# Kernel tuning notes

Measured on AMD Instinct MI355X. Metric: run time of the kernel, lower is better.

## Reference

```python
import jax, jax.numpy as jnp
import numpy as np

B, S, H = 8, 1024, 1024
NH, DH = 16, 64
F_DIM, E, TOPK = 4096, 8, 2
EPS = 1e-5


def setup_inputs() -> dict:
    key = jax.random.key(0)
    ks = jax.random.split(key, 12)
    s = 0.02
    return {
        "x": jax.random.normal(ks[0], (B, S, H), jnp.float32),
        "ln1_w": jnp.ones((H,), jnp.float32),
        "ln1_b": jnp.zeros((H,), jnp.float32),
        "ln2_w": jnp.ones((H,), jnp.float32),
        "ln2_b": jnp.zeros((H,), jnp.float32),
        "in_proj_w": jax.random.normal(ks[1], (3 * H, H), jnp.float32) * s,
        "in_proj_b": jnp.zeros((3 * H,), jnp.float32),
        "out_proj_w": jax.random.normal(ks[2], (H, H), jnp.float32) * s,
        "out_proj_b": jnp.zeros((H,), jnp.float32),
        "gate_w": jax.random.normal(ks[3], (E, H), jnp.float32) * s,
        "gate_b": jnp.zeros((E,), jnp.float32),
        "w1": jax.random.normal(ks[4], (E, H, F_DIM), jnp.float32) * s,
        "b1": jnp.zeros((E, F_DIM), jnp.float32),
        "w2": jax.random.normal(ks[5], (E, F_DIM, H), jnp.float32) * s,
        "b2": jnp.zeros((E, H), jnp.float32),
    }


def _layernorm(x, w, b):
    mu = jnp.mean(x, axis=-1, keepdims=True)
    var = jnp.var(x, axis=-1, keepdims=True)
    return (x - mu) * jax.lax.rsqrt(var + EPS) * w + b


def reference(x, ln1_w, ln1_b, ln2_w, ln2_b, in_proj_w, in_proj_b,
              out_proj_w, out_proj_b, gate_w, gate_b, w1, b1, w2, b2):
    # --- attention sub-block ---
    xn = _layernorm(x, ln1_w, ln1_b)
    qkv = xn @ in_proj_w.T + in_proj_b                     # [B,S,3H]
    q, k, v = jnp.split(qkv, 3, axis=-1)
    q = q.reshape(B, S, NH, DH).transpose(0, 2, 1, 3)      # [B,NH,S,DH]
    k = k.reshape(B, S, NH, DH).transpose(0, 2, 1, 3)
    v = v.reshape(B, S, NH, DH).transpose(0, 2, 1, 3)
    scores = jnp.einsum("bhqd,bhkd->bhqk", q, k) / jnp.sqrt(jnp.float32(DH))
    attn = jax.nn.softmax(scores, axis=-1)
    ctx = jnp.einsum("bhqk,bhkd->bhqd", attn, v)
    ctx = ctx.transpose(0, 2, 1, 3).reshape(B, S, H)
    x = x + ctx @ out_proj_w.T + out_proj_b

    # --- MoE sub-block (dense compute-all-experts, top-k combine) ---
    xn2 = _layernorm(x, ln2_w, ln2_b)
    logits = xn2 @ gate_w.T + gate_b                       # [B,S,E]
    topk_vals, topk_idx = jax.lax.top_k(logits, TOPK)      # [B,S,K]
    probs = jax.nn.softmax(topk_vals, axis=-1)
    hid = jax.nn.gelu(jnp.einsum("bsh,ehf->bsef", xn2, w1) + b1, approximate=False)
    expert_out = jnp.einsum("bsef,efh->bseh", hid, w2) + b2  # [B,S,E,H]
    selected = jnp.take_along_axis(expert_out, topk_idx[..., None], axis=2)  # [B,S,K,H]
    moe_out = jnp.sum(probs[..., None] * selected, axis=2)
    return x + moe_out
```

## Files before the change

kernel.cpp:

```cpp
#include <hip/hip_runtime.h>
#include <math.h>

typedef unsigned short u16;
typedef short short8 __attribute__((ext_vector_type(8)));
typedef float f32x4 __attribute__((ext_vector_type(4)));
typedef unsigned short us4 __attribute__((ext_vector_type(4)));

#define NTOK 8192
#define NEXP 8

__device__ __forceinline__ u16 f2bf(float f) {
  union { float f; unsigned u; } v; v.f = f;
  unsigned r = v.u + 0x7FFFu + ((v.u >> 16) & 1u);
  return (u16)(r >> 16);
}

__global__ void cast_kernel(const float* __restrict__ in, u16* __restrict__ out, int n4) {
  int i = blockIdx.x * blockDim.x + threadIdx.x;
  if (i < n4) {
    float4 v = ((const float4*)in)[i];
    us4 o;
    o[0] = f2bf(v.x); o[1] = f2bf(v.y); o[2] = f2bf(v.z); o[3] = f2bf(v.w);
    ((us4*)out)[i] = o;
  }
}

__global__ void transpose_cast(const float* __restrict__ in, u16* __restrict__ out, int R, int C) {
  __shared__ float tile[32][33];
  const size_t eoff = (size_t)blockIdx.z * (size_t)R * (size_t)C;
  in += eoff; out += eoff;
  int tx = threadIdx.x & 31, ty = threadIdx.x >> 5;
  int rb = blockIdx.y * 32, cb = blockIdx.x * 32;
#pragma unroll
  for (int p = 0; p < 4; ++p)
    tile[ty + p*8][tx] = in[(size_t)(rb + ty + p*8) * C + (cb + tx)];
  __syncthreads();
#pragma unroll
  for (int p = 0; p < 4; ++p)
    out[(size_t)(cb + ty + p*8) * R + (rb + tx)] = f2bf(tile[tx][ty + p*8]);
}

__global__ void ln1_kernel(const float* __restrict__ x, const float* __restrict__ w,
                           const float* __restrict__ b, u16* __restrict__ xn) {
  const int t = blockIdx.x, tid = threadIdx.x;
  __shared__ float red[8];
  float4 v = ((const float4*)(x + (size_t)t * 1024))[tid];
  float s  = v.x + v.y + v.z + v.w;
  float sq = v.x*v.x + v.y*v.y + v.z*v.z + v.w*v.w;
#pragma unroll
  for (int m = 1; m < 64; m <<= 1) { s += __shfl_xor(s, m, 64); sq += __shfl_xor(sq, m, 64); }
  if ((tid & 63) == 0) { red[tid >> 6] = s; red[4 + (tid >> 6)] = sq; }
  __syncthreads();
  float S = red[0] + red[1] + red[2] + red[3];
  float Q = red[4] + red[5] + red[6] + red[7];
  float mu  = S * (1.0f / 1024.0f);
  float var = Q * (1.0f / 1024.0f) - mu * mu;
  float inv = rsqrtf(var + 1e-5f);
  float4 wv = ((const float4*)w)[tid];
  float4 bv = ((const float4*)b)[tid];
  us4 o;
  o[0] = f2bf((v.x - mu) * inv * wv.x + bv.x);
  o[1] = f2bf((v.y - mu) * inv * wv.y + bv.y);
  o[2] = f2bf((v.z - mu) * inv * wv.z + bv.z);
  o[3] = f2bf((v.w - mu) * inv * wv.w + bv.w);
  ((us4*)(xn + (size_t)t * 1024))[tid] = o;
}

__global__ void ln2_gate_kernel(const float* __restrict__ x2, const float* __restrict__ w,
                                const float* __restrict__ b, const float* __restrict__ gw,
                                const float* __restrict__ gb, u16* __restrict__ xn2,
                                int* __restrict__ cnt, int* __restrict__ list_tok,
                                float* __restrict__ list_prob) {
  const int t = blockIdx.x, tid = threadIdx.x;
  __shared__ float red[8];
  __shared__ float logits[NEXP];
  __shared__ float xrow[1024];
  float4 v = ((const float4*)(x2 + (size_t)t * 1024))[tid];
  float s  = v.x + v.y + v.z + v.w;
  float sq = v.x*v.x + v.y*v.y + v.z*v.z + v.w*v.w;
#pragma unroll
  for (int m = 1; m < 64; m <<= 1) { s += __shfl_xor(s, m, 64); sq += __shfl_xor(sq, m, 64); }
  if ((tid & 63) == 0) { red[tid >> 6] = s; red[4 + (tid >> 6)] = sq; }
  __syncthreads();
  float S = red[0] + red[1] + red[2] + red[3];
  float Q = red[4] + red[5] + red[6] + red[7];
  float mu  = S * (1.0f / 1024.0f);
  float var = Q * (1.0f / 1024.0f) - mu * mu;
  float inv = rsqrtf(var + 1e-5f);
  float4 wv = ((const float4*)w)[tid];
  float4 bv = ((const float4*)b)[tid];
  float n0 = (v.x - mu) * inv * wv.x + bv.x;
  float n1 = (v.y - mu) * inv * wv.y + bv.y;
  float n2 = (v.z - mu) * inv * wv.z + bv.z;
  float n3 = (v.w - mu) * inv * wv.w + bv.w;
  xrow[tid*4+0] = n0; xrow[tid*4+1] = n1; xrow[tid*4+2] = n2; xrow[tid*4+3] = n3;
  us4 o; o[0] = f2bf(n0); o[1] = f2bf(n1); o[2] = f2bf(n2); o[3] = f2bf(n3);
  ((us4*)(xn2 + (size_t)t * 1024))[tid] = o;
  __syncthreads();
  int e = tid >> 5, l32 = tid & 31;
  const float* gwe = gw + e * 1024;
  float part = 0.0f;
  for (int i = l32; i < 1024; i += 32) part += xrow[i] * gwe[i];
#pragma unroll
  for (int m = 1; m < 32; m <<= 1) part += __shfl_xor(part, m, 64);
  if (l32 == 0) logits[e] = part + gb[e];
  __syncthreads();
  if (tid == 0) {
    float v0 = -1e30f; int e0 = 0;
#pragma unroll
    for (int i = 0; i < NEXP; ++i) { float L = logits[i]; if (L > v0) { v0 = L; e0 = i; } }
    float v1 = -1e30f; int e1 = 0;
#pragma unroll
    for (int i = 0; i < NEXP; ++i) { if (i == e0) continue; float L = logits[i]; if (L > v1) { v1 = L; e1 = i; } }
    float texp = expf(v1 - v0);
    float p0 = 1.0f / (1.0f + texp);
    float p1 = texp / (1.0f + texp);
    int s0 = atomicAdd(&cnt[e0], 1);
    list_tok[e0 * NTOK + s0] = t; list_prob[e0 * NTOK + s0] = p0;
    int s1 = atomicAdd(&cnt[e1], 1);
    list_tok[e1 * NTOK + s1] = t; list_prob[e1 * NTOK + s1] = p1;
  }
}

__launch_bounds__(256)
__global__ void attn_kernel(const u16* __restrict__ qkv, u16* __restrict__ ctx) {
  const int bh = blockIdx.y;
  const int b = bh >> 4, h = bh & 15;
  const int q0 = blockIdx.x * 64;
  const int tokBase = b * 1024;
  __shared__ __align__(16) u16 Qs[64 * 72];
  __shared__ __align__(16) u16 Ks[64 * 72];
  __shared__ __align__(16) u16 Vts[64 * 72];
  __shared__ __align__(16) u16 Ps[64 * 72];
  const int tid = threadIdx.x;
  const int wave = tid >> 6, lane = tid & 63, g = lane >> 4, lr = lane & 15;

  {
    int r = tid >> 2, d0 = (tid & 3) * 16;
    const u16* src = qkv + (size_t)(tokBase + q0 + r) * 3072 + h * 64 + d0;
    *(short8*)&Qs[r * 72 + d0]     = *(const short8*)src;
    *(short8*)&Qs[r * 72 + d0 + 8] = *(const short8*)(src + 8);
  }
  __syncthreads();
  short8 aq0 = *(const short8*)&Qs[(wave * 16 + lr) * 72 + g * 8];
  short8 aq1 = *(const short8*)&Qs[(wave * 16 + lr) * 72 + 32 + g * 8];

  const f32x4 zf = {0.f, 0.f, 0.f, 0.f};
  f32x4 Ofr[4] = {zf, zf, zf, zf};
  float m_run[4], l_run[4];
#pragma unroll
  for (int r = 0; r < 4; ++r) { m_run[r] = -1e30f; l_run[r] = 0.f; }

  for (int kt = 0; kt < 1024; kt += 64) {
    __syncthreads();
    {
      int r = tid >> 2, d0 = (tid & 3) * 16;
      const u16* ksrc = qkv + (size_t)(tokBase + kt + r) * 3072 + 1024 + h * 64 + d0;
      *(short8*)&Ks[r * 72 + d0]     = *(const short8*)ksrc;
      *(short8*)&Ks[r * 72 + d0 + 8] = *(const short8*)(ksrc + 8);
      const u16* vsrc = qkv + (size_t)(tokBase + kt + r) * 3072 + 2048 + h * 64 + d0;
      short8 v0 = *(const short8*)vsrc, v1 = *(const short8*)(vsrc + 8);
#pragma unroll
      for (int j = 0; j < 8; ++j) Vts[(d0 + j) * 72 + r] = (u16)v0[j];
#pragma unroll
      for (int j = 0; j < 8; ++j) Vts[(d0 + 8 + j) * 72 + r] = (u16)v1[j];
    }
    __syncthreads();
    f32x4 sf[4];
#pragma unroll
    for (int n = 0; n < 4; ++n) sf[n] = zf;
#pragma unroll
    for (int n = 0; n < 4; ++n) {
      short8 bk0 = *(const short8*)&Ks[(n * 16 + lr) * 72 + g * 8];
      short8 bk1 = *(const short8*)&Ks[(n * 16 + lr) * 72 + 32 + g * 8];
      sf[n] = __builtin_amdgcn_mfma_f32_16x16x32_bf16(aq0, bk0, sf[n], 0, 0, 0);
      sf[n] = __builtin_amdgcn_mfma_f32_16x16x32_bf16(aq1, bk1, sf[n], 0, 0, 0);
    }
#pragma unroll
    for (int n = 0; n < 4; ++n)
#pragma unroll
      for (int r = 0; r < 4; ++r) sf[n][r] *= 0.125f;
    float mnew[4], sc[4];
#pragma unroll
    for (int r = 0; r < 4; ++r) {
      float t0 = fmaxf(fmaxf(sf[0][r], sf[1][r]), fmaxf(sf[2][r], sf[3][r]));
#pragma unroll
      for (int msk = 1; msk < 16; msk <<= 1) t0 = fmaxf(t0, __shfl_xor(t0, msk, 64));
      mnew[r] = fmaxf(m_run[r], t0);
      sc[r] = __expf(m_run[r] - mnew[r]);
      m_run[r] = mnew[r];
    }
#pragma unroll
    for (int n = 0; n < 4; ++n)
#pragma unroll
      for (int r = 0; r < 4; ++r) sf[n][r] = __expf(sf[n][r] - mnew[r]);
#pragma unroll
    for (int r = 0; r < 4; ++r) {
      float s0 = sf[0][r] + sf[1][r] + sf[2][r] + sf[3][r];
#pragma unroll
      for (int msk = 1; msk < 16; msk <<= 1) s0 += __shfl_xor(s0, msk, 64);
      l_run[r] = l_run[r] * sc[r] + s0;
    }
#pragma unroll
    for (int nd = 0; nd < 4; ++nd)
#pragma unroll
      for (int r = 0; r < 4; ++r) Ofr[nd][r] *= sc[r];
#pragma unroll
    for (int n = 0; n < 4; ++n)
#pragma unroll
      for (int r = 0; r < 4; ++r)
        Ps[(wave * 16 + g * 4 + r) * 72 + n * 16 + lr] = f2bf(sf[n][r]);
    __syncthreads();
    short8 ap0 = *(const short8*)&Ps[(wave * 16 + lr) * 72 + g * 8];
    short8 ap1 = *(const short8*)&Ps[(wave * 16 + lr) * 72 + 32 + g * 8];
#pragma unroll
    for (int nd = 0; nd < 4; ++nd) {
      short8 bv0 = *(const short8*)&Vts[(nd * 16 + lr) * 72 + g * 8];
      short8 bv1 = *(const short8*)&Vts[(nd * 16 + lr) * 72 + 32 + g * 8];
      Ofr[nd] = __builtin_amdgcn_mfma_f32_16x16x32_bf16(ap0, bv0, Ofr[nd], 0, 0, 0);
      Ofr[nd] = __builtin_amdgcn_mfma_f32_16x16x32_bf16(ap1, bv1, Ofr[nd], 0, 0, 0);
    }
  }
#pragma unroll
  for (int nd = 0; nd < 4; ++nd)
#pragma unroll
    for (int r = 0; r < 4; ++r) {
      int tok = tokBase + q0 + wave * 16 + g * 4 + r;
      int col = h * 64 + nd * 16 + lr;
      ctx[(size_t)tok * 1024 + col] = f2bf(Ofr[nd][r] / l_run[r]);
    }
}

template<int EPI>
__launch_bounds__(256)
__global__ void gemm128(const u16* __restrict__ Abase, const u16* __restrict__ Bbase,
                        int K, int lda, int N, int ldc,
                        const float* __restrict__ bias,
                        const float* __restrict__ resid,
                        float* __restrict__ outF,
                        u16* __restrict__ outB,
                        const int* __restrict__ cnt,
                        const int* __restrict__ list_tok,
                        const float* __restrict__ list_prob) {
  const int tid = threadIdx.x;
  const int wave = tid >> 6, lane = tid & 63, g = lane >> 4, lr = lane & 15;
  const int n0 = blockIdx.x * 128;
  const int m0 = blockIdx.y * 128;
  const int e  = blockIdx.z;

  int M = NTOK;
  int slotBase = 0;
  const u16* Bw = Bbase;
  const float* biasp = bias;
  if constexpr (EPI == 2 || EPI == 3) {
    for (int j = 0; j < e; ++j) slotBase += cnt[j];
    M = cnt[e];
    if (m0 >= M) return;
    Bw += (size_t)e * (size_t)N * (size_t)K;
    biasp = bias + (size_t)e * N;
  }

  __shared__ __align__(16) u16 As[128 * 64];
  __shared__ __align__(16) u16 Bs[128 * 64];
  char* AsB = (char*)As;
  char* BsB = (char*)Bs;

  size_t aOff[4], bOff[4];
#pragma unroll
  for (int i = 0; i < 4; ++i) {
    int grp = i * 256 + tid;
    int r = grp >> 3;
    int ce = (grp & 7) * 8;
    int arow;
    if constexpr (EPI == 2) {
      int ridx = m0 + r; if (ridx > M - 1) ridx = M - 1;
      arow = list_tok[e * NTOK + ridx];
    } else if constexpr (EPI == 3) {
      int ridx = m0 + r; if (ridx > M - 1) ridx = M - 1;
      arow = slotBase + ridx;
    } else {
      arow = m0 + r;
    }
    aOff[i] = (size_t)arow * (size_t)lda + (size_t)ce;
    bOff[i] = (size_t)(n0 + r) * (size_t)K + (size_t)ce;
  }

  const f32x4 zf = {0.f, 0.f, 0.f, 0.f};
  f32x4 acc[4][4];
#pragma unroll
  for (int m = 0; m < 4; ++m)
#pragma unroll
    for (int n = 0; n < 4; ++n) acc[m][n] = zf;

  const int wm = wave >> 1, wn = wave & 1;

  for (int kt = 0; kt < K; kt += 64) {
#pragma unroll
    for (int i = 0; i < 4; ++i)
      __builtin_amdgcn_global_load_lds(
        (const __attribute__((address_space(1))) unsigned int*)(const void*)(Abase + aOff[i] + kt),
        (__attribute__((address_space(3))) unsigned int*)(void*)(AsB + (i * 256 + wave * 64) * 16),
        16, 0, 0);
#pragma unroll
    for (int i = 0; i < 4; ++i)
      __builtin_amdgcn_global_load_lds(
        (const __attribute__((address_space(1))) unsigned int*)(const void*)(Bw + bOff[i] + kt),
        (__attribute__((address_space(3))) unsigned int*)(void*)(BsB + (i * 256 + wave * 64) * 16),
        16, 0, 0);
    __syncthreads();
    short8 af[4][2], bfr[4][2];
#pragma unroll
    for (int m = 0; m < 4; ++m)
#pragma unroll
      for (int kk = 0; kk < 2; ++kk)
        af[m][kk] = *(const short8*)&As[(wm * 64 + m * 16 + lr) * 64 + kk * 32 + g * 8];
#pragma unroll
    for (int n = 0; n < 4; ++n)
#pragma unroll
      for (int kk = 0; kk < 2; ++kk)
        bfr[n][kk] = *(const short8*)&Bs[(wn * 64 + n * 16 + lr) * 64 + kk * 32 + g * 8];
#pragma unroll
    for (int kk = 0; kk < 2; ++kk)
#pragma unroll
      for (int m = 0; m < 4; ++m)
#pragma unroll
        for (int n = 0; n < 4; ++n)
          acc[m][n] = __builtin_amdgcn_mfma_f32_16x16x32_bf16(af[m][kk], bfr[n][kk], acc[m][n], 0, 0, 0);
    __syncthreads();
  }

#pragma unroll
  for (int m = 0; m < 4; ++m) {
    int rloc = wm * 64 + m * 16 + g * 4;
#pragma unroll
    for (int n = 0; n < 4; ++n) {
      int gc = n0 + wn * 64 + n * 16 + lr;
      float bcol = biasp[gc];
#pragma unroll
      for (int r = 0; r < 4; ++r) {
        int ridx = m0 + rloc + r;
        float vv = acc[m][n][r] + bcol;
        if constexpr (EPI == 0) {
          outB[(size_t)ridx * ldc + gc] = f2bf(vv);
        } else if constexpr (EPI == 1) {
          size_t off = (size_t)ridx * ldc + gc;
          outF[off] = vv + resid[off];
        } else if constexpr (EPI == 2) {
          if (ridx < M)
            outB[(size_t)(slotBase + ridx) * ldc + gc] =
              f2bf(0.5f * vv * (1.0f + erff(vv * 0.70710678f)));
        } else {
          if (ridx < M) {
            int tok = list_tok[e * NTOK + ridx];
            float p = list_prob[e * NTOK + ridx];
            atomicAdd(&outF[(size_t)tok * ldc + gc], vv * p);
          }
        }
      }
    }
  }
}

extern "C" void kernel_launch(void* const* d_in, const int* in_sizes, int n_in,
                              void* d_out, int out_size, void* d_ws, size_t ws_size,
                              hipStream_t stream) {
  const float* x    = (const float*)d_in[0];
  const float* ln1w = (const float*)d_in[1];
  const float* ln1b = (const float*)d_in[2];
  const float* ln2w = (const float*)d_in[3];
  const float* ln2b = (const float*)d_in[4];
  const float* inw  = (const float*)d_in[5];
  const float* inb  = (const float*)d_in[6];
  const float* outw = (const float*)d_in[7];
  const float* outb = (const float*)d_in[8];
  const float* gw   = (const float*)d_in[9];
  const float* gb   = (const float*)d_in[10];
  const float* w1   = (const float*)d_in[11];
  const float* b1   = (const float*)d_in[12];
  const float* w2   = (const float*)d_in[13];
  const float* b2   = (const float*)d_in[14];
  float* out = (float*)d_out;
  char* ws = (char*)d_ws;

  u16* xn1 = (u16*)(ws + 0);
  u16* qkv = (u16*)(ws + 16777216);
  u16* ctx = (u16*)(ws + 67108864);
  u16* hid = (u16*)(ws + 0);
  u16* xn2 = (u16*)(ws + 134217728);
  u16* w1t = (u16*)(ws + 150994944);
  u16* winb  = (u16*)(ws + 218103808);
  u16* woutb = (u16*)(ws + 224395264);
  int*   cnt  = (int*)(ws + 226492416);
  int*   ltok = (int*)(ws + 226492672);
  float* lprb = (float*)(ws + 226754816);
  bool lateW2 = ws_size < 294125824ull;
  u16* w2t = lateW2 ? (u16*)(ws + 134217728) : (u16*)(ws + 227016960);

  cast_kernel<<<3072, 256, 0, stream>>>(inw, winb, 786432);
  cast_kernel<<<1024, 256, 0, stream>>>(outw, woutb, 262144);
  transpose_cast<<<dim3(128, 32, 8), 256, 0, stream>>>(w1, w1t, 1024, 4096);
  if (!lateW2) transpose_cast<<<dim3(32, 128, 8), 256, 0, stream>>>(w2, w2t, 4096, 1024);

  ln1_kernel<<<8192, 256, 0, stream>>>(x, ln1w, ln1b, xn1);
  gemm128<0><<<dim3(24, 64, 1), 256, 0, stream>>>(xn1, winb, 1024, 1024, 3072, 3072,
                                                  inb, nullptr, nullptr, qkv, nullptr, nullptr, nullptr);
  attn_kernel<<<dim3(16, 128), 256, 0, stream>>>(qkv, ctx);
  gemm128<1><<<dim3(8, 64, 1), 256, 0, stream>>>(ctx, woutb, 1024, 1024, 1024, 1024,
                                                 outb, x, out, nullptr, nullptr, nullptr, nullptr);

  hipMemsetAsync(cnt, 0, 32, stream);
  ln2_gate_kernel<<<8192, 256, 0, stream>>>(out, ln2w, ln2b, gw, gb, xn2, cnt, ltok, lprb);
  gemm128<2><<<dim3(32, 64, 8), 256, 0, stream>>>(xn2, w1t, 1024, 1024, 4096, 4096,
                                                  b1, nullptr, nullptr, hid, cnt, ltok, lprb);
  if (lateW2) transpose_cast<<<dim3(32, 128, 8), 256, 0, stream>>>(w2, w2t, 4096, 1024);
  gemm128<3><<<dim3(8, 64, 8), 256, 0, stream>>>(hid, w2t, 4096, 4096, 1024, 1024,
                                                 b2, nullptr, out, nullptr, cnt, ltok, lprb);
}
```

Before: 1.317 ms.

## Use 256x256 double-buffered GEMM tiles, XCD remap, and atomic-free MoE combine

The 128x128 single-buffered GEMM becomes a 256x256 tile, 512-thread kernel. It adds double-buffered LDS stages with global_load_lds prefetching, XOR-swizzled LDS layout, s_setprio around MFMA bursts, and a workgroup remap that groups neighbouring tiles onto the same XCD. The weight transpose now uses 64x64 tiles with vectorized reads and writes. When workspace allows, the second expert GEMM writes bf16 partial outputs that a combine kernel reduces per token using a token-to-slot map, replacing float atomics on the output. The larger tiles raise register and LDS pressure, and the combine adds an extra pass and bf16 rounding of expert outputs.

```diff
diff --git a/kernel.cpp b/kernel.cpp
--- a/kernel.cpp
+++ b/kernel.cpp
@@ -13,6 +13,14 @@
   union { float f; unsigned u; } v; v.f = f;
   unsigned r = v.u + 0x7FFFu + ((v.u >> 16) & 1u);
   return (u16)(r >> 16);
+}
+__device__ __forceinline__ float bf2f(u16 u) {
+  union { unsigned u; float f; } v; v.u = ((unsigned)u) << 16; return v.f;
+}
+__device__ __forceinline__ void gload16(const u16* src, u16* ldsDst) {
+  __builtin_amdgcn_global_load_lds(
+    (const __attribute__((address_space(1))) unsigned int*)(const void*)src,
+    (__attribute__((address_space(3))) unsigned int*)(void*)ldsDst, 16, 0, 0);
 }
 
 __global__ void cast_kernel(const float* __restrict__ in, u16* __restrict__ out, int n4) {
@@ -26,18 +34,32 @@
 }
 
 __global__ void transpose_cast(const float* __restrict__ in, u16* __restrict__ out, int R, int C) {
-  __shared__ float tile[32][33];
+  __shared__ float tile[64][65];
   const size_t eoff = (size_t)blockIdx.z * (size_t)R * (size_t)C;
   in += eoff; out += eoff;
-  int tx = threadIdx.x & 31, ty = threadIdx.x >> 5;
-  int rb = blockIdx.y * 32, cb = blockIdx.x * 32;
-#pragma unroll
-  for (int p = 0; p < 4; ++p)
-    tile[ty + p*8][tx] = in[(size_t)(rb + ty + p*8) * C + (cb + tx)];
-  __syncthreads();
-#pragma unroll
-  for (int p = 0; p < 4; ++p)
-    out[(size_t)(cb + ty + p*8) * R + (rb + tx)] = f2bf(tile[tx][ty + p*8]);
+  const int rb = blockIdx.y * 64, cb = blockIdx.x * 64;
+  const int tid = threadIdx.x;
+  const int lr4 = tid >> 4;
+  const int lc4 = (tid & 15) * 4;
+#pragma unroll
+  for (int p = 0; p < 4; ++p) {
+    float4 v = *(const float4*)&in[(size_t)(rb + p * 16 + lr4) * C + cb + lc4];
+    tile[p * 16 + lr4][lc4 + 0] = v.x;
+    tile[p * 16 + lr4][lc4 + 1] = v.y;
+    tile[p * 16 + lr4][lc4 + 2] = v.z;
+    tile[p * 16 + lr4][lc4 + 3] = v.w;
+  }
+  __syncthreads();
+  const int oc = tid >> 3;
+  const int orr = (tid & 7) * 8;
+#pragma unroll
+  for (int p = 0; p < 2; ++p) {
+    int c = p * 32 + oc;
+    short8 o;
+#pragma unroll
+    for (int j = 0; j < 8; ++j) o[j] = (short)f2bf(tile[orr + j][c]);
+    *(short8*)&out[(size_t)(cb + c) * R + rb + orr] = o;
+  }
 }
 
 __global__ void ln1_kernel(const float* __restrict__ x, const float* __restrict__ w,
@@ -70,7 +92,7 @@
                                 const float* __restrict__ b, const float* __restrict__ gw,
                                 const float* __restrict__ gb, u16* __restrict__ xn2,
                                 int* __restrict__ cnt, int* __restrict__ list_tok,
-                                float* __restrict__ list_prob) {
+                                float* __restrict__ list_prob, int* __restrict__ tok2slot) {
   const int t = blockIdx.x, tid = threadIdx.x;
   __shared__ float red[8];
   __shared__ float logits[NEXP];
@@ -119,6 +141,10 @@
     list_tok[e0 * NTOK + s0] = t; list_prob[e0 * NTOK + s0] = p0;
     int s1 = atomicAdd(&cnt[e1], 1);
     list_tok[e1 * NTOK + s1] = t; list_prob[e1 * NTOK + s1] = p1;
+    if (tok2slot) {
+      tok2slot[2 * t]     = e0 * NTOK + s0;
+      tok2slot[2 * t + 1] = e1 * NTOK + s1;
+    }
   }
 }
 
@@ -232,8 +258,8 @@
 }
 
 template<int EPI>
-__launch_bounds__(256)
-__global__ void gemm128(const u16* __restrict__ Abase, const u16* __restrict__ Bbase,
+__launch_bounds__(512, 2)
+__global__ void gemm256(const u16* __restrict__ Abase, const u16* __restrict__ Bbase,
                         int K, int lda, int N, int ldc,
                         const float* __restrict__ bias,
                         const float* __restrict__ resid,
@@ -242,17 +268,21 @@
                         const int* __restrict__ cnt,
                         const int* __restrict__ list_tok,
                         const float* __restrict__ list_prob) {
-  const int tid = threadIdx.x;
-  const int wave = tid >> 6, lane = tid & 63, g = lane >> 4, lr = lane & 15;
-  const int n0 = blockIdx.x * 128;
-  const int m0 = blockIdx.y * 128;
-  const int e  = blockIdx.z;
+  const int gx = gridDim.x, gy = gridDim.y;
+  int nwg = gx * gy * gridDim.z;
+  int orig = blockIdx.x + blockIdx.y * gx + blockIdx.z * gx * gy;
+  int q8 = nwg >> 3, r8 = nwg & 7, xcd = orig & 7, lid = orig >> 3;
+  int wg = (xcd < r8 ? xcd * (q8 + 1) : r8 * (q8 + 1) + (xcd - r8) * q8) + lid;
+  const int bz = wg / (gx * gy); int rem = wg - bz * gx * gy;
+  const int n0 = (rem % gx) * 256;
+  const int m0 = (rem / gx) * 256;
+  const int e  = bz;
 
   int M = NTOK;
   int slotBase = 0;
   const u16* Bw = Bbase;
   const float* biasp = bias;
-  if constexpr (EPI == 2 || EPI == 3) {
+  if constexpr (EPI >= 2) {
     for (int j = 0; j < e; ++j) slotBase += cnt[j];
     M = cnt[e];
     if (m0 >= M) return;
@@ -260,78 +290,98 @@
     biasp = bias + (size_t)e * N;
   }
 
-  __shared__ __align__(16) u16 As[128 * 64];
-  __shared__ __align__(16) u16 Bs[128 * 64];
-  char* AsB = (char*)As;
-  char* BsB = (char*)Bs;
-
-  size_t aOff[4], bOff[4];
+  __shared__ __align__(16) u16 As[2 * 16384];
+  __shared__ __align__(16) u16 Bs[2 * 16384];
+
+  const int tid = threadIdx.x;
+  const int wave = tid >> 6, lane = tid & 63, g = lane >> 4, lr = lane & 15;
+  const int wm = wave >> 2, wn = wave & 3;
+
+  size_t aoff[4], boff[4];
 #pragma unroll
   for (int i = 0; i < 4; ++i) {
-    int grp = i * 256 + tid;
-    int r = grp >> 3;
-    int ce = (grp & 7) * 8;
+    int ci = i * 512 + tid;
+    int row = ci >> 3, c = ci & 7;
+    int lc = c ^ (row & 7);
     int arow;
     if constexpr (EPI == 2) {
-      int ridx = m0 + r; if (ridx > M - 1) ridx = M - 1;
+      int ridx = m0 + row; if (ridx > M - 1) ridx = M - 1;
       arow = list_tok[e * NTOK + ridx];
-    } else if constexpr (EPI == 3) {
-      int ridx = m0 + r; if (ridx > M - 1) ridx = M - 1;
+    } else if constexpr (EPI >= 3) {
+      int ridx = m0 + row; if (ridx > M - 1) ridx = M - 1;
       arow = slotBase + ridx;
     } else {
-      arow = m0 + r;
-    }
-    aOff[i] = (size_t)arow * (size_t)lda + (size_t)ce;
-    bOff[i] = (size_t)(n0 + r) * (size_t)K + (size_t)ce;
-  }
+      arow = m0 + row;
+    }
+    aoff[i] = (size_t)arow * (size_t)lda + (size_t)(lc << 3);
+    boff[i] = (size_t)(n0 + row) * (size_t)K + (size_t)(lc << 3);
+  }
+
+  const int NT = K >> 6;
+
+#define STAGE(T) do { int _t = (T); if (_t < NT) { int _b = (_t & 1) << 14; int _kt = _t << 6; \
+    _Pragma("unroll") for (int i = 0; i < 4; ++i) \
+      gload16(Abase + aoff[i] + _kt, &As[_b + ((i * 512 + wave * 64) << 3)]); \
+    _Pragma("unroll") for (int i = 0; i < 4; ++i) \
+      gload16(Bw + boff[i] + _kt, &Bs[_b + ((i * 512 + wave * 64) << 3)]); } } while (0)
+
+  const int sw = lr & 7;
+  const int abase = (wm * 128 + lr) * 64;
+  const int bbase = (wn * 64 + lr) * 64;
+  const int sk0 = (g ^ sw) * 8;
+  const int sk1 = ((4 + g) ^ sw) * 8;
 
   const f32x4 zf = {0.f, 0.f, 0.f, 0.f};
-  f32x4 acc[4][4];
-#pragma unroll
-  for (int m = 0; m < 4; ++m)
+  f32x4 acc[8][4];
+#pragma unroll
+  for (int m = 0; m < 8; ++m)
 #pragma unroll
     for (int n = 0; n < 4; ++n) acc[m][n] = zf;
 
-  const int wm = wave >> 1, wn = wave & 1;
-
-  for (int kt = 0; kt < K; kt += 64) {
-#pragma unroll
-    for (int i = 0; i < 4; ++i)
-      __builtin_amdgcn_global_load_lds(
-        (const __attribute__((address_space(1))) unsigned int*)(const void*)(Abase + aOff[i] + kt),
-        (__attribute__((address_space(3))) unsigned int*)(void*)(AsB + (i * 256 + wave * 64) * 16),
-        16, 0, 0);
-#pragma unroll
-    for (int i = 0; i < 4; ++i)
-      __builtin_amdgcn_global_load_lds(
-        (const __attribute__((address_space(1))) unsigned int*)(const void*)(Bw + bOff[i] + kt),
-        (__attribute__((address_space(3))) unsigned int*)(void*)(BsB + (i * 256 + wave * 64) * 16),
-        16, 0, 0);
-    __syncthreads();
-    short8 af[4][2], bfr[4][2];
-#pragma unroll
-    for (int m = 0; m < 4; ++m)
-#pragma unroll
-      for (int kk = 0; kk < 2; ++kk)
-        af[m][kk] = *(const short8*)&As[(wm * 64 + m * 16 + lr) * 64 + kk * 32 + g * 8];
-#pragma unroll
-    for (int n = 0; n < 4; ++n)
-#pragma unroll
-      for (int kk = 0; kk < 2; ++kk)
-        bfr[n][kk] = *(const short8*)&Bs[(wn * 64 + n * 16 + lr) * 64 + kk * 32 + g * 8];
-#pragma unroll
-    for (int kk = 0; kk < 2; ++kk)
-#pragma unroll
-      for (int m = 0; m < 4; ++m)
-#pragma unroll
-        for (int n = 0; n < 4; ++n)
-          acc[m][n] = __builtin_amdgcn_mfma_f32_16x16x32_bf16(af[m][kk], bfr[n][kk], acc[m][n], 0, 0, 0);
-    __syncthreads();
-  }
-
-#pragma unroll
-  for (int m = 0; m < 4; ++m) {
-    int rloc = wm * 64 + m * 16 + g * 4;
+  STAGE(0);
+  STAGE(1);
+
+  for (int t = 0; t < NT; ++t) {
+    if (t < NT - 1) { asm volatile("s_waitcnt vmcnt(8)" ::: "memory"); }
+    else           { asm volatile("s_waitcnt vmcnt(0)" ::: "memory"); }
+    __builtin_amdgcn_s_barrier();
+    asm volatile("" ::: "memory");
+    const u16* Ab = As + ((t & 1) << 14);
+    const u16* Bb = Bs + ((t & 1) << 14);
+    short8 bfr[2][4];
+#pragma unroll
+    for (int n = 0; n < 4; ++n) bfr[0][n] = *(const short8*)&Bb[bbase + n * 1024 + sk0];
+#pragma unroll
+    for (int n = 0; n < 4; ++n) bfr[1][n] = *(const short8*)&Bb[bbase + n * 1024 + sk1];
+    short8 afr[8];
+#pragma unroll
+    for (int m = 0; m < 8; ++m) afr[m] = *(const short8*)&Ab[abase + m * 1024 + sk0];
+    __builtin_amdgcn_s_setprio(1);
+#pragma unroll
+    for (int m = 0; m < 8; ++m)
+#pragma unroll
+      for (int n = 0; n < 4; ++n)
+        acc[m][n] = __builtin_amdgcn_mfma_f32_16x16x32_bf16(afr[m], bfr[0][n], acc[m][n], 0, 0, 0);
+    __builtin_amdgcn_s_setprio(0);
+#pragma unroll
+    for (int m = 0; m < 8; ++m) afr[m] = *(const short8*)&Ab[abase + m * 1024 + sk1];
+    asm volatile("s_waitcnt lgkmcnt(0)" ::: "memory");
+    __builtin_amdgcn_s_barrier();
+    asm volatile("" ::: "memory");
+    STAGE(t + 2);
+    __builtin_amdgcn_s_setprio(1);
+#pragma unroll
+    for (int m = 0; m < 8; ++m)
+#pragma unroll
+      for (int n = 0; n < 4; ++n)
+        acc[m][n] = __builtin_amdgcn_mfma_f32_16x16x32_bf16(afr[m], bfr[1][n], acc[m][n], 0, 0, 0);
+    __builtin_amdgcn_s_setprio(0);
+  }
+#undef STAGE
+
+#pragma unroll
+  for (int m = 0; m < 8; ++m) {
+    int rloc = wm * 128 + m * 16 + g * 4;
 #pragma unroll
     for (int n = 0; n < 4; ++n) {
       int gc = n0 + wn * 64 + n * 16 + lr;
@@ -349,6 +399,9 @@
           if (ridx < M)
             outB[(size_t)(slotBase + ridx) * ldc + gc] =
               f2bf(0.5f * vv * (1.0f + erff(vv * 0.70710678f)));
+        } else if constexpr (EPI == 3) {
+          if (ridx < M)
+            outB[(size_t)(slotBase + ridx) * ldc + gc] = f2bf(vv);
         } else {
           if (ridx < M) {
             int tok = list_tok[e * NTOK + ridx];
@@ -359,6 +412,31 @@
       }
     }
   }
+}
+
+__global__ void combine_kernel(const u16* __restrict__ part, const int* __restrict__ cnt,
+                               const int* __restrict__ tok2slot, const float* __restrict__ lprb,
+                               float* __restrict__ out) {
+  const int t = blockIdx.x, tid = threadIdx.x;
+  __shared__ int base[NEXP];
+  if (tid == 0) {
+    int b = 0;
+#pragma unroll
+    for (int j = 0; j < NEXP; ++j) { base[j] = b; b += cnt[j]; }
+  }
+  __syncthreads();
+  int c0 = tok2slot[2 * t], c1 = tok2slot[2 * t + 1];
+  float p0 = lprb[c0], p1 = lprb[c1];
+  int g0 = base[c0 >> 13] + (c0 & 8191);
+  int g1 = base[c1 >> 13] + (c1 & 8191);
+  us4 a = ((const us4*)(part + (size_t)g0 * 1024))[tid];
+  us4 b = ((const us4*)(part + (size_t)g1 * 1024))[tid];
+  float4 o = ((const float4*)(out + (size_t)t * 1024))[tid];
+  o.x += p0 * bf2f(a[0]) + p1 * bf2f(b[0]);
+  o.y += p0 * bf2f(a[1]) + p1 * bf2f(b[1]);
+  o.z += p0 * bf2f(a[2]) + p1 * bf2f(b[2]);
+  o.w += p0 * bf2f(a[3]) + p1 * bf2f(b[3]);
+  ((float4*)(out + (size_t)t * 1024))[tid] = o;
 }
 
 extern "C" void kernel_launch(void* const* d_in, const int* in_sizes, int n_in,
@@ -390,29 +468,45 @@
   u16* w1t = (u16*)(ws + 150994944);
   u16* winb  = (u16*)(ws + 218103808);
   u16* woutb = (u16*)(ws + 224395264);
-  int*   cnt  = (int*)(ws + 226492416);
-  int*   ltok = (int*)(ws + 226492672);
-  float* lprb = (float*)(ws + 226754816);
-  bool lateW2 = ws_size < 294125824ull;
-  u16* w2t = lateW2 ? (u16*)(ws + 134217728) : (u16*)(ws + 227016960);
+  u16* w2t = (u16*)(ws + 134217728);
+  u16* part = (u16*)(ws + 201326592);
+
+  const bool bigWS = ws_size >= 235471872ull;
+  int*   cnt, *ltok, *t2s; float* lprb;
+  if (bigWS) {
+    cnt  = (int*)(ws + 234881024);
+    ltok = (int*)(ws + 234882048);
+    lprb = (float*)(ws + 235144192);
+    t2s  = (int*)(ws + 235406336);
+  } else {
+    cnt  = (int*)(ws + 226492416);
+    ltok = (int*)(ws + 226492672);
+    lprb = (float*)(ws + 226754816);
+    t2s  = nullptr;
+  }
 
   cast_kernel<<<3072, 256, 0, stream>>>(inw, winb, 786432);
   cast_kernel<<<1024, 256, 0, stream>>>(outw, woutb, 262144);
-  transpose_cast<<<dim3(128, 32, 8), 256, 0, stream>>>(w1, w1t, 1024, 4096);
-  if (!lateW2) transpose_cast<<<dim3(32, 128, 8), 256, 0, stream>>>(w2, w2t, 4096, 1024);
+  transpose_cast<<<dim3(64, 16, 8), 256, 0, stream>>>(w1, w1t, 1024, 4096);
 
   ln1_kernel<<<8192, 256, 0, stream>>>(x, ln1w, ln1b, xn1);
-  gemm128<0><<<dim3(24, 64, 1), 256, 0, stream>>>(xn1, winb, 1024, 1024, 3072, 3072,
+  gemm256<0><<<dim3(12, 32, 1), 512, 0, stream>>>(xn1, winb, 1024, 1024, 3072, 3072,
                                                   inb, nullptr, nullptr, qkv, nullptr, nullptr, nullptr);
   attn_kernel<<<dim3(16, 128), 256, 0, stream>>>(qkv, ctx);
-  gemm128<1><<<dim3(8, 64, 1), 256, 0, stream>>>(ctx, woutb, 1024, 1024, 1024, 1024,
+  gemm256<1><<<dim3(4, 32, 1), 512, 0, stream>>>(ctx, woutb, 1024, 1024, 1024, 1024,
                                                  outb, x, out, nullptr, nullptr, nullptr, nullptr);
 
   hipMemsetAsync(cnt, 0, 32, stream);
-  ln2_gate_kernel<<<8192, 256, 0, stream>>>(out, ln2w, ln2b, gw, gb, xn2, cnt, ltok, lprb);
-  gemm128<2><<<dim3(32, 64, 8), 256, 0, stream>>>(xn2, w1t, 1024, 1024, 4096, 4096,
+  ln2_gate_kernel<<<8192, 256, 0, stream>>>(out, ln2w, ln2b, gw, gb, xn2, cnt, ltok, lprb, t2s);
+  gemm256<2><<<dim3(16, 32, 8), 512, 0, stream>>>(xn2, w1t, 1024, 1024, 4096, 4096,
                                                   b1, nullptr, nullptr, hid, cnt, ltok, lprb);
-  if (lateW2) transpose_cast<<<dim3(32, 128, 8), 256, 0, stream>>>(w2, w2t, 4096, 1024);
-  gemm128<3><<<dim3(8, 64, 8), 256, 0, stream>>>(hid, w2t, 4096, 4096, 1024, 1024,
-                                                 b2, nullptr, out, nullptr, cnt, ltok, lprb);
-}
+  transpose_cast<<<dim3(16, 64, 8), 256, 0, stream>>>(w2, w2t, 4096, 1024);
+  if (bigWS) {
+    gemm256<3><<<dim3(4, 32, 8), 512, 0, stream>>>(hid, w2t, 4096, 4096, 1024, 1024,
+                                                   b2, nullptr, nullptr, part, cnt, ltok, lprb);
+    combine_kernel<<<8192, 256, 0, stream>>>(part, cnt, t2s, lprb, out);
+  } else {
+    gemm256<4><<<dim3(4, 32, 8), 512, 0, stream>>>(hid, w2t, 4096, 4096, 1024, 1024,
+                                                   b2, nullptr, out, nullptr, cnt, ltok, lprb);
+  }
+}
```

New measurement: 1.082 ms. -17.8%, faster.
